# Kernel optimization log

Measured on AMD Instinct MI355X. Metric: run time of the kernel, lower is better.

## Reference

```python
import jax, jax.numpy as jnp
import numpy as np

NUM_LABELS = 64
START, END, PAD = 0, 1, 2
B, L, V, D = 128, 1024, 30000, 256


def make_transitions(key):
    # replicates CRF.init_weights
    t = jax.random.uniform(key, (NUM_LABELS, NUM_LABELS), minval=-0.1, maxval=0.1)
    t = t.at[:, START].set(-10000.0)
    t = t.at[END, :].set(-10000.0)
    t = t.at[PAD, :].set(-10000.0)
    t = t.at[:, PAD].set(-10000.0)
    t = t.at[PAD, PAD].set(0.0)
    t = t.at[PAD, END].set(0.0)
    return t.astype(jnp.float32)


def setup_inputs() -> dict:
    key = jax.random.key(0)
    k0, k1, k2, k3, k4 = jax.random.split(key, 5)
    x = jax.random.randint(k0, (B, L), 0, V)
    tags = jax.random.randint(k1, (B, L), 0, NUM_LABELS)
    mask = jnp.ones((B, L), dtype=jnp.float32)  # ignored by CRF (source passes mask=None)
    embed = jax.random.normal(k2, (V, D), dtype=jnp.float32)
    W = jax.random.normal(k3, (D, NUM_LABELS), dtype=jnp.float32) * 0.05
    b = jnp.zeros((NUM_LABELS,), dtype=jnp.float32)
    trans = make_transitions(k4)
    return {"x": x, "tags": tags, "mask": mask, "embed": embed, "W": W, "b": b, "trans": trans}


def _crf_nll(emissions, tags, trans):
    # emissions: [B, L, T]; tags: [B, L]; trans: [T, T]
    # NOTE: original CRF.forward ignores the user mask (passes mask=None ->
    # all-ones mask), so every position is valid and last tag is tags[:, -1].
    # gold path score
    e_scores = jnp.take_along_axis(emissions, tags[:, :, None], axis=2)[:, :, 0].sum(axis=1)
    t_scores = trans[tags[:, :-1], tags[:, 1:]].sum(axis=1)
    scores = e_scores + t_scores + trans[START, tags[:, 0]] + trans[tags[:, -1], END]
    # log partition: forward algorithm (log-space recursion over time)
    alpha0 = trans[START][None, :] + emissions[:, 0]  # [B, T]

    def step(alphas, emit_t):
        # alphas: [B, T_prev] -> logsumexp over previous tag
        new = jax.nn.logsumexp(alphas[:, :, None] + trans[None, :, :], axis=1) + emit_t
        return new, None

    alphas, _ = jax.lax.scan(step, alpha0, jnp.swapaxes(emissions[:, 1:], 0, 1))
    log_z = jax.nn.logsumexp(alphas + trans[:, END][None, :], axis=1)  # [B]
    return -jnp.sum(scores - log_z)


def reference(x, tags, mask, embed, W, b, trans):
    emissions = embed[x] @ W + b  # [B, L, T]
    return _crf_nll(emissions, tags, trans)
```

## Files before the change

kernel.cpp:

```cpp
#include <hip/hip_runtime.h>
#include <hip/hip_bf16.h>

#define B_ 128
#define L_ 1024
#define T_ 64
#define CSH 5
#define C_ 32

using short8 = __attribute__((ext_vector_type(8))) short;
using f32x4  = __attribute__((ext_vector_type(4))) float;
using f32x16 = __attribute__((ext_vector_type(16))) float;

static __device__ __forceinline__ unsigned short bfb(float x) {
  return __builtin_bit_cast(unsigned short, __float2bfloat16(x));
}
static __device__ __forceinline__ float asf(unsigned u) { return __builtin_bit_cast(float, u); }
static __device__ __forceinline__ float bf2f(unsigned short b) { return asf(((unsigned)b) << 16); }
static __device__ __forceinline__ unsigned pk2(float lo, float hi) {
  __hip_bfloat162 h = __float22bfloat162_rn(float2{lo, hi});
  unsigned u;
  __builtin_memcpy(&u, &h, 4);
  return u;
}
static __device__ __forceinline__ unsigned pk2t(float lo, float hi) {
  return __builtin_amdgcn_perm(__builtin_bit_cast(unsigned, hi),
                               __builtin_bit_cast(unsigned, lo), 0x07060302u);
}
static __device__ __forceinline__ void pswap(unsigned& x, unsigned& y) {
  asm("v_permlane32_swap_b32 %0, %1" : "+v"(x), "+v"(y));
}

__global__ __launch_bounds__(256) void k_prep(const float* __restrict__ W,
                                              unsigned short* __restrict__ Wswz,
                                              float* __restrict__ score,
                                              float* __restrict__ out) {
  if (blockIdx.x == 0) {
    if (threadIdx.x < 128) score[threadIdx.x] = 0.f;
    if (threadIdx.x == 0) out[0] = 0.f;
  }
  const int t = blockIdx.x * 256 + threadIdx.x;
  const int e = t * 4, k = e >> 6, n0 = e & 63;
  float4 w4 = *(const float4*)(W + e);
  const int base = ((k >> 5) << 11) + ((n0 >> 4) << 9) + (((k >> 3) & 3) << 7) +
                   ((n0 & 15) << 3) + (k & 7);
  Wswz[base + 0]  = bfb(w4.x);
  Wswz[base + 8]  = bfb(w4.y);
  Wswz[base + 16] = bfb(w4.z);
  Wswz[base + 24] = bfb(w4.w);
}

__global__ __launch_bounds__(256) void k_scan(const int* __restrict__ x,
                                              const int* __restrict__ tags,
                                              const float* __restrict__ embed,
                                              const unsigned short* __restrict__ Wswz,
                                              const float* __restrict__ bias,
                                              const float* __restrict__ trans,
                                              unsigned short* __restrict__ XT,
                                              float* __restrict__ rlog,
                                              float* __restrict__ score) {
  __shared__ __align__(16) unsigned short Ftile[4][2048];
  const int wv = threadIdx.x >> 6, L = threadIdx.x & 63;
  const int job = blockIdx.x * 4 + wv;
  const int c = job & (C_ - 1);
  const int b = job >> CSH;
  const int K = (1023 + C_ - 1) >> CSH;
  const int a = 1 + c * K;
  const int len = min(K, 1024 - a);
  const int nh = L & 31, hh = L >> 5;
  const int m = L & 15, q = L >> 4;
  unsigned short* Ft = Ftile[wv];
  const int* tg = tags + (size_t)b * L_;

  const float bj0 = bias[m], bj1 = bias[16 + m], bj2 = bias[32 + m], bj3 = bias[48 + m];
  for (int p = 0; p < 2; p++) {
    int tok = a + 16 * p + m;
    if (tok > 1023) tok = 1023;
    const float* er = embed + (size_t)x[b * 1024 + tok] * 256;
    f32x4 acc[4] = {{0.f,0.f,0.f,0.f},{0.f,0.f,0.f,0.f},{0.f,0.f,0.f,0.f},{0.f,0.f,0.f,0.f}};
#pragma unroll
    for (int kap = 0; kap < 8; kap++) {
      float4 p0 = *(const float4*)(er + 32 * kap + 8 * q);
      float4 p1 = *(const float4*)(er + 32 * kap + 8 * q + 4);
      unsigned u0 = pk2(p0.x, p0.y), u1 = pk2(p0.z, p0.w);
      unsigned u2 = pk2(p1.x, p1.y), u3 = pk2(p1.z, p1.w);
      short8 af = __builtin_bit_cast(short8, make_uint4(u0, u1, u2, u3));
#pragma unroll
      for (int u = 0; u < 4; u++) {
        short8 bf8 = *(const short8*)&Wswz[kap * 2048 + u * 512 + q * 128 + m * 8];
        acc[u] = __builtin_amdgcn_mfma_f32_16x16x32_bf16(af, bf8, acc[u], 0, 0, 0);
      }
    }
#pragma unroll
    for (int r = 0; r < 4; r++) {
      float e0 = acc[0][r] + bj0, e1 = acc[1][r] + bj1;
      float e2 = acc[2][r] + bj2, e3 = acc[3][r] + bj3;
      float mr = fmaxf(fmaxf(e0, e1), fmaxf(e2, e3));
#pragma unroll
      for (int off = 1; off < 16; off <<= 1) mr = fmaxf(mr, __shfl_xor(mr, off));
      float x0 = __expf(e0 - mr), x1 = __expf(e1 - mr);
      float x2 = __expf(e2 - mr), x3 = __expf(e3 - mr);
      float sr = (x0 + x1) + (x2 + x3);
#pragma unroll
      for (int off = 1; off < 16; off <<= 1) sr += __shfl_xor(sr, off);
      float rs = 1.0f / sr;
      const int row = 16 * p + 4 * q + r;
      Ft[row * 64 + m]      = bfb(x0 * rs);
      Ft[row * 64 + 16 + m] = bfb(x1 * rs);
      Ft[row * 64 + 32 + m] = bfb(x2 * rs);
      Ft[row * 64 + 48 + m] = bfb(x3 * rs);
    }
  }
  {
    float gold = 0.f;
    if (L < len) {
      const int tga = tg[a + L], tgp = tg[a - 1 + L];
      gold = __logf(bf2f(Ft[L * 64 + tga])) + trans[tgp * T_ + tga];
    }
#pragma unroll
    for (int off = 1; off < 64; off <<= 1) gold += __shfl_xor(gold, off);
    if (L == 0) atomicAdd(&score[b], gold);
  }

  short8 Af[2][4];
#pragma unroll
  for (int I = 0; I < 2; I++)
#pragma unroll
    for (int kap = 0; kap < 4; kap++) {
      short8 aa;
#pragma unroll
      for (int d = 0; d < 8; d++) {
        const int k = 16 * kap + 8 * hh + d;
        aa[d] = (short)bfb(__expf(trans[k * T_ + 32 * I + nh]));
      }
      Af[I][kap] = aa;
    }
  unsigned Bf[4][2][4];
#pragma unroll
  for (int kap = 0; kap < 4; kap++)
#pragma unroll
    for (int J = 0; J < 2; J++)
#pragma unroll
      for (int dw = 0; dw < 4; dw++) {
        int k0 = 16 * kap + 8 * hh + 2 * dw, n = 32 * J + nh;
        unsigned u = 0;
        if (k0 == n) u = 0x3F80u;
        if (k0 + 1 == n) u = 0x3F800000u;
        Bf[kap][J][dw] = u;
      }

  float logacc = 0.f;
  const f32x16 Z = {};
  for (int s = 0; s < len; s++) {
    uint2 Fc[2][4];
#pragma unroll
    for (int I = 0; I < 2; I++)
#pragma unroll
      for (int j = 0; j < 4; j++)
        Fc[I][j] = *(const uint2*)&Ft[s * 64 + (16 * I + 4 * j + 2 * hh) * 2];
    const bool rn = ((s & 15) == 15);
    float rs = 1.0f;
#pragma unroll
    for (int J = 0; J < 2; J++) {
      f32x16 D[2];
#pragma unroll
      for (int I = 0; I < 2; I++) {
        short8 b0 = __builtin_bit_cast(short8,
            make_uint4(Bf[0][J][0], Bf[0][J][1], Bf[0][J][2], Bf[0][J][3]));
        f32x16 d = __builtin_amdgcn_mfma_f32_32x32x16_bf16(Af[I][0], b0, Z, 0, 0, 0);
#pragma unroll
        for (int kap = 1; kap < 4; kap++) {
          short8 bk = __builtin_bit_cast(short8,
              make_uint4(Bf[kap][J][0], Bf[kap][J][1], Bf[kap][J][2], Bf[kap][J][3]));
          d = __builtin_amdgcn_mfma_f32_32x32x16_bf16(Af[I][kap], bk, d, 0, 0, 0);
        }
        D[I] = d;
      }
#pragma unroll
      for (int I = 0; I < 2; I++)
#pragma unroll
        for (int j = 0; j < 4; j++) {
          uint2 g = Fc[I][j];
          float f0 = asf(g.x << 16), f1 = asf(g.x & 0xffff0000u);
          float f2 = asf(g.y << 16), f3 = asf(g.y & 0xffff0000u);
          D[I][4 * j + 0] *= f0;
          D[I][4 * j + 1] *= f1;
          D[I][4 * j + 2] *= f2;
          D[I][4 * j + 3] *= f3;
        }
      if (rn) {
        if (J == 0) {
          float mx = D[0][0];
#pragma unroll
          for (int I = 0; I < 2; I++)
#pragma unroll
            for (int r = 0; r < 16; r++) mx = fmaxf(mx, D[I][r]);
#pragma unroll
          for (int off = 1; off < 64; off <<= 1) mx = fmaxf(mx, __shfl_xor(mx, off));
          rs = 1.0f / mx;
          logacc += __logf(mx);
        }
#pragma unroll
        for (int I = 0; I < 2; I++)
#pragma unroll
          for (int r = 0; r < 16; r++) D[I][r] *= rs;
      }
      unsigned PDt[2][4][2];
#pragma unroll
      for (int I = 0; I < 2; I++)
#pragma unroll
        for (int j = 0; j < 4; j++) {
          PDt[I][j][0] = pk2t(D[I][4 * j + 0], D[I][4 * j + 1]);
          PDt[I][j][1] = pk2t(D[I][4 * j + 2], D[I][4 * j + 3]);
        }
      if (s == len - 1) {
        unsigned short* Xrow = XT + (size_t)job * 4096 + 32 * J + nh;
#pragma unroll
        for (int I = 0; I < 2; I++)
#pragma unroll
          for (int j = 0; j < 4; j++)
#pragma unroll
            for (int pp = 0; pp < 2; pp++) {
              const int r = 32 * I + 8 * j + 4 * hh + 2 * pp;
              Xrow[(size_t)r * 64] = (unsigned short)(PDt[I][j][pp] & 0xffffu);
              Xrow[(size_t)(r + 1) * 64] = (unsigned short)(PDt[I][j][pp] >> 16);
            }
      } else {
#pragma unroll
        for (int kap = 0; kap < 4; kap++) {
          const int Ip = kap >> 1, e2 = 2 * (kap & 1);
          unsigned x0 = PDt[Ip][e2][0], y0 = PDt[Ip][e2 + 1][0];
          unsigned x1 = PDt[Ip][e2][1], y1 = PDt[Ip][e2 + 1][1];
          pswap(x0, y0);
          pswap(x1, y1);
          Bf[kap][J][0] = x0;
          Bf[kap][J][1] = x1;
          Bf[kap][J][2] = y0;
          Bf[kap][J][3] = y1;
        }
      }
    }
  }
  if (L == 0) rlog[job] = logacc;
}

__global__ __launch_bounds__(256) void k_tail(const unsigned short* __restrict__ XT,
                                              const float* __restrict__ rlog,
                                              const float* __restrict__ score,
                                              const int* __restrict__ x,
                                              const float* __restrict__ embed,
                                              const float* __restrict__ W,
                                              const float* __restrict__ bias,
                                              const float* __restrict__ trans,
                                              const int* __restrict__ tags,
                                              float* __restrict__ out) {
  __shared__ __align__(16) unsigned short Ptile[4][4096];
  __shared__ __align__(16) float vS[64];
  __shared__ float tlg[4];
  const int wv = threadIdx.x >> 6, L = threadIdx.x & 63;
  const int b = blockIdx.x;
  const int nh = L & 31, hh = L >> 5;
  const int* tg = tags + (size_t)b * L_;
  const f32x16 Z = {};
  unsigned Bf[4][2][4];

  const unsigned short* Sb = XT + (size_t)b * C_ * 4096;
  {
    float plog = 0.f;
#pragma unroll
    for (int kap = 0; kap < 4; kap++)
#pragma unroll
      for (int J = 0; J < 2; J++)
#pragma unroll
        for (int dw = 0; dw < 4; dw++) {
          int k0 = 16 * kap + 8 * hh + 2 * dw, n = 32 * J + nh;
          unsigned u = 0;
          if (k0 == n) u = 0x3F80u;
          if (k0 + 1 == n) u = 0x3F800000u;
          Bf[kap][J][dw] = u;
        }
    for (int r = 0; r < 8; r++) {
      short8 Ap[2][4];
#pragma unroll
      for (int I = 0; I < 2; I++)
#pragma unroll
        for (int kap = 0; kap < 4; kap++)
          Ap[I][kap] = *(const short8*)(Sb + (size_t)(8 * wv + r) * 4096 +
                                        (32 * I + nh) * 64 + 16 * kap + 8 * hh);
      const bool last = (r == 7);
      float rsw = 1.0f;
#pragma unroll
      for (int J = 0; J < 2; J++) {
        f32x16 D[2];
#pragma unroll
        for (int I = 0; I < 2; I++) {
          short8 b0 = __builtin_bit_cast(short8,
              make_uint4(Bf[0][J][0], Bf[0][J][1], Bf[0][J][2], Bf[0][J][3]));
          f32x16 d = __builtin_amdgcn_mfma_f32_32x32x16_bf16(Ap[I][0], b0, Z, 0, 0, 0);
#pragma unroll
          for (int kap = 1; kap < 4; kap++) {
            short8 bk = __builtin_bit_cast(short8,
                make_uint4(Bf[kap][J][0], Bf[kap][J][1], Bf[kap][J][2], Bf[kap][J][3]));
            d = __builtin_amdgcn_mfma_f32_32x32x16_bf16(Ap[I][kap], bk, d, 0, 0, 0);
          }
          D[I] = d;
        }
        if (J == 0) {
          float mx = D[0][0];
#pragma unroll
          for (int I = 0; I < 2; I++)
#pragma unroll
            for (int rr = 0; rr < 16; rr++) mx = fmaxf(mx, D[I][rr]);
#pragma unroll
          for (int off = 1; off < 64; off <<= 1) mx = fmaxf(mx, __shfl_xor(mx, off));
          mx = fmaxf(mx, 1e-30f);
          rsw = 1.0f / mx;
          plog += __logf(mx);
        }
#pragma unroll
        for (int I = 0; I < 2; I++)
#pragma unroll
          for (int rr = 0; rr < 16; rr++) D[I][rr] *= rsw;
        unsigned PDt[2][4][2];
#pragma unroll
        for (int I = 0; I < 2; I++)
#pragma unroll
          for (int j = 0; j < 4; j++) {
            PDt[I][j][0] = pk2t(D[I][4 * j + 0], D[I][4 * j + 1]);
            PDt[I][j][1] = pk2t(D[I][4 * j + 2], D[I][4 * j + 3]);
          }
        if (last) {
          unsigned short* Xrow = Ptile[wv] + 32 * J + nh;
#pragma unroll
          for (int I = 0; I < 2; I++)
#pragma unroll
            for (int j = 0; j < 4; j++)
#pragma unroll
              for (int pp = 0; pp < 2; pp++) {
                const int rr = 32 * I + 8 * j + 4 * hh + 2 * pp;
                Xrow[rr * 64] = (unsigned short)(PDt[I][j][pp] & 0xffffu);
                Xrow[(rr + 1) * 64] = (unsigned short)(PDt[I][j][pp] >> 16);
              }
        } else {
#pragma unroll
          for (int kap = 0; kap < 4; kap++) {
            const int Ip = kap >> 1, e2 = 2 * (kap & 1);
            unsigned x0 = PDt[Ip][e2][0], y0 = PDt[Ip][e2 + 1][0];
            unsigned x1 = PDt[Ip][e2][1], y1 = PDt[Ip][e2 + 1][1];
            pswap(x0, y0);
            pswap(x1, y1);
            Bf[kap][J][0] = x0;
            Bf[kap][J][1] = x1;
            Bf[kap][J][2] = y0;
            Bf[kap][J][3] = y1;
          }
        }
      }
    }
    if (L == 0) tlg[wv] = plog;
  }
  __syncthreads();
  if (threadIdx.x >= 64) return;

  float tlog = (tlg[0] + tlg[1]) + (tlg[2] + tlg[3]);
  {
#pragma unroll
    for (int kap = 0; kap < 4; kap++)
#pragma unroll
      for (int J = 0; J < 2; J++)
#pragma unroll
        for (int dw = 0; dw < 4; dw++) {
          int k0 = 16 * kap + 8 * hh + 2 * dw, n = 32 * J + nh;
          unsigned u = 0;
          if (k0 == n) u = 0x3F80u;
          if (k0 + 1 == n) u = 0x3F800000u;
          Bf[kap][J][dw] = u;
        }
    for (int r = 0; r < 4; r++) {
      short8 Ap[2][4];
#pragma unroll
      for (int I = 0; I < 2; I++)
#pragma unroll
        for (int kap = 0; kap < 4; kap++)
          Ap[I][kap] = *(const short8*)&Ptile[r][(32 * I + nh) * 64 + 16 * kap + 8 * hh];
      const bool last = (r == 3);
      float rsw = 1.0f;
#pragma unroll
      for (int J = 0; J < 2; J++) {
        f32x16 D[2];
#pragma unroll
        for (int I = 0; I < 2; I++) {
          short8 b0 = __builtin_bit_cast(short8,
              make_uint4(Bf[0][J][0], Bf[0][J][1], Bf[0][J][2], Bf[0][J][3]));
          f32x16 d = __builtin_amdgcn_mfma_f32_32x32x16_bf16(Ap[I][0], b0, Z, 0, 0, 0);
#pragma unroll
          for (int kap = 1; kap < 4; kap++) {
            short8 bk = __builtin_bit_cast(short8,
                make_uint4(Bf[kap][J][0], Bf[kap][J][1], Bf[kap][J][2], Bf[kap][J][3]));
            d = __builtin_amdgcn_mfma_f32_32x32x16_bf16(Ap[I][kap], bk, d, 0, 0, 0);
          }
          D[I] = d;
        }
        if (J == 0) {
          float mx = D[0][0];
#pragma unroll
          for (int I = 0; I < 2; I++)
#pragma unroll
            for (int rr = 0; rr < 16; rr++) mx = fmaxf(mx, D[I][rr]);
#pragma unroll
          for (int off = 1; off < 64; off <<= 1) mx = fmaxf(mx, __shfl_xor(mx, off));
          mx = fmaxf(mx, 1e-30f);
          rsw = 1.0f / mx;
          tlog += __logf(mx);
        }
#pragma unroll
        for (int I = 0; I < 2; I++)
#pragma unroll
          for (int rr = 0; rr < 16; rr++) D[I][rr] *= rsw;
        unsigned PDt[2][4][2];
#pragma unroll
        for (int I = 0; I < 2; I++)
#pragma unroll
          for (int j = 0; j < 4; j++) {
            PDt[I][j][0] = pk2t(D[I][4 * j + 0], D[I][4 * j + 1]);
            PDt[I][j][1] = pk2t(D[I][4 * j + 2], D[I][4 * j + 3]);
          }
        if (last) {
          unsigned short* Xrow = Ptile[0] + 32 * J + nh;
#pragma unroll
          for (int I = 0; I < 2; I++)
#pragma unroll
            for (int j = 0; j < 4; j++)
#pragma unroll
              for (int pp = 0; pp < 2; pp++) {
                const int rr = 32 * I + 8 * j + 4 * hh + 2 * pp;
                Xrow[rr * 64] = (unsigned short)(PDt[I][j][pp] & 0xffffu);
                Xrow[(rr + 1) * 64] = (unsigned short)(PDt[I][j][pp] >> 16);
              }
        } else {
#pragma unroll
          for (int kap = 0; kap < 4; kap++) {
            const int Ip = kap >> 1, e2 = 2 * (kap & 1);
            unsigned x0 = PDt[Ip][e2][0], y0 = PDt[Ip][e2 + 1][0];
            unsigned x1 = PDt[Ip][e2][1], y1 = PDt[Ip][e2 + 1][1];
            pswap(x0, y0);
            pswap(x1, y1);
            Bf[kap][J][0] = x0;
            Bf[kap][J][1] = x1;
            Bf[kap][J][2] = y0;
            Bf[kap][J][3] = y1;
          }
        }
      }
    }
  }

  const int i = L;
  const float* er0 = embed + (size_t)x[(size_t)b * L_] * 256;
  float e0 = bias[i], e1 = 0.f, e2 = 0.f, e3 = 0.f;
#pragma unroll 16
  for (int d = 0; d < 256; d += 4) {
    e0 = fmaf(er0[d + 0], W[(d + 0) * T_ + i], e0);
    e1 = fmaf(er0[d + 1], W[(d + 1) * T_ + i], e1);
    e2 = fmaf(er0[d + 2], W[(d + 2) * T_ + i], e2);
    e3 = fmaf(er0[d + 3], W[(d + 3) * T_ + i], e3);
  }
  float e = (e0 + e1) + (e2 + e3);
  float mr = e;
#pragma unroll
  for (int off = 1; off < 64; off <<= 1) mr = fmaxf(mr, __shfl_xor(mr, off));
  float pex = __expf(e - mr);
  float sr = pex;
#pragma unroll
  for (int off = 1; off < 64; off <<= 1) sr += __shfl_xor(sr, off);
  const int t0 = tg[0];
  float sc = score[b];
  sc += (__shfl(e, t0) - mr) - __logf(sr);
  sc += trans[t0] + trans[tg[L_ - 1] * T_ + 1];
  vS[i] = __expf(trans[i]) * (pex / sr);
  float rl = (i < 32) ? rlog[b * C_ + i] : 0.f;
#pragma unroll
  for (int off = 1; off < 64; off <<= 1) rl += __shfl_xor(rl, off);
  const uint4* Zr = (const uint4*)Ptile[0];
  uint4 Xr[8];
#pragma unroll
  for (int t = 0; t < 8; t++) Xr[t] = Zr[i * 8 + t];
  float a0 = 0.f, a1 = 0.f, a2 = 0.f, a3 = 0.f;
#pragma unroll
  for (int t = 0; t < 8; t++) {
    float4 va = *(const float4*)&vS[8 * t];
    float4 vb = *(const float4*)&vS[8 * t + 4];
    a0 = fmaf(asf(Xr[t].x << 16), va.x, a0);
    a1 = fmaf(asf(Xr[t].x & 0xffff0000u), va.y, a1);
    a2 = fmaf(asf(Xr[t].y << 16), va.z, a2);
    a3 = fmaf(asf(Xr[t].y & 0xffff0000u), va.w, a3);
    a0 = fmaf(asf(Xr[t].z << 16), vb.x, a0);
    a1 = fmaf(asf(Xr[t].z & 0xffff0000u), vb.y, a1);
    a2 = fmaf(asf(Xr[t].w << 16), vb.z, a2);
    a3 = fmaf(asf(Xr[t].w & 0xffff0000u), vb.w, a3);
  }
  float t2 = ((a0 + a1) + (a2 + a3)) * __expf(trans[i * T_ + 1]);
#pragma unroll
  for (int off = 1; off < 64; off <<= 1) t2 += __shfl_xor(t2, off);
  if (i == 0) {
    const float logz = rl + tlog + __logf(t2);
    atomicAdd(out, -(sc - logz));
  }
}

extern "C" void kernel_launch(void* const* d_in, const int* in_sizes, int n_in,
                              void* d_out, int out_size, void* d_ws, size_t ws_size,
                              hipStream_t stream) {
  const int* x = (const int*)d_in[0];
  const int* tags = (const int*)d_in[1];
  const float* embed = (const float*)d_in[3];
  const float* W = (const float*)d_in[4];
  const float* bias = (const float*)d_in[5];
  const float* trans = (const float*)d_in[6];

  char* ws = (char*)d_ws;
  unsigned short* XT = (unsigned short*)ws;
  float* rlog = (float*)(ws + (size_t)C_ * 1048576);
  float* score = (float*)((char*)rlog + 4096 * 4);
  unsigned short* Wswz = (unsigned short*)((char*)score + 128 * 4);
  float* out = (float*)d_out;

  k_prep<<<16, 256, 0, stream>>>(W, Wswz, score, out);
  k_scan<<<32 * C_, 256, 0, stream>>>(x, tags, embed, Wswz, bias, trans, XT, rlog, score);
  k_tail<<<B_, 256, 0, stream>>>(XT, rlog, score, x, embed, W, bias, trans, tags, out);
}
```

Baseline: 196.1 us.

## Store chunk products in MFMA B-fragment layout and combine chunks in reverse order

The scan kernel now writes each chunk's final transfer matrix as packed B-operand register fragments with coalesced uint4 stores, replacing scattered 2-byte transposed stores. The tail kernel combines chunks from last to first, using stored fragments directly as A operands with register double-buffered prefetch. The final vector product is folded into the last MFMA step, which removes the separate LDS readback. This relies on the reversed multiplication order and the reinterpreted layout being mathematically equivalent, and adds register pressure from the prefetch buffers.

```diff
diff --git a/kernel.cpp b/kernel.cpp
--- a/kernel.cpp
+++ b/kernel.cpp
@@ -55,7 +55,7 @@
                                               const unsigned short* __restrict__ Wswz,
                                               const float* __restrict__ bias,
                                               const float* __restrict__ trans,
-                                              unsigned short* __restrict__ XT,
+                                              uint4* __restrict__ XT,
                                               float* __restrict__ rlog,
                                               float* __restrict__ score) {
   __shared__ __align__(16) unsigned short Ftile[4][2048];
@@ -212,38 +212,33 @@
           PDt[I][j][0] = pk2t(D[I][4 * j + 0], D[I][4 * j + 1]);
           PDt[I][j][1] = pk2t(D[I][4 * j + 2], D[I][4 * j + 3]);
         }
-      if (s == len - 1) {
-        unsigned short* Xrow = XT + (size_t)job * 4096 + 32 * J + nh;
-#pragma unroll
-        for (int I = 0; I < 2; I++)
-#pragma unroll
-          for (int j = 0; j < 4; j++)
-#pragma unroll
-            for (int pp = 0; pp < 2; pp++) {
-              const int r = 32 * I + 8 * j + 4 * hh + 2 * pp;
-              Xrow[(size_t)r * 64] = (unsigned short)(PDt[I][j][pp] & 0xffffu);
-              Xrow[(size_t)(r + 1) * 64] = (unsigned short)(PDt[I][j][pp] >> 16);
-            }
-      } else {
-#pragma unroll
-        for (int kap = 0; kap < 4; kap++) {
-          const int Ip = kap >> 1, e2 = 2 * (kap & 1);
-          unsigned x0 = PDt[Ip][e2][0], y0 = PDt[Ip][e2 + 1][0];
-          unsigned x1 = PDt[Ip][e2][1], y1 = PDt[Ip][e2 + 1][1];
-          pswap(x0, y0);
-          pswap(x1, y1);
-          Bf[kap][J][0] = x0;
-          Bf[kap][J][1] = x1;
-          Bf[kap][J][2] = y0;
-          Bf[kap][J][3] = y1;
-        }
-      }
-    }
+#pragma unroll
+      for (int kap = 0; kap < 4; kap++) {
+        const int Ip = kap >> 1, e2 = 2 * (kap & 1);
+        unsigned x0 = PDt[Ip][e2][0], y0 = PDt[Ip][e2 + 1][0];
+        unsigned x1 = PDt[Ip][e2][1], y1 = PDt[Ip][e2 + 1][1];
+        pswap(x0, y0);
+        pswap(x1, y1);
+        Bf[kap][J][0] = x0;
+        Bf[kap][J][1] = x1;
+        Bf[kap][J][2] = y0;
+        Bf[kap][J][3] = y1;
+      }
+    }
+  }
+  {
+    uint4* Xj = XT + (size_t)job * 512 + L;
+#pragma unroll
+    for (int J = 0; J < 2; J++)
+#pragma unroll
+      for (int kap = 0; kap < 4; kap++)
+        Xj[(J * 4 + kap) * 64] =
+            make_uint4(Bf[kap][J][0], Bf[kap][J][1], Bf[kap][J][2], Bf[kap][J][3]);
   }
   if (L == 0) rlog[job] = logacc;
 }
 
-__global__ __launch_bounds__(256) void k_tail(const unsigned short* __restrict__ XT,
+__global__ __launch_bounds__(256) void k_tail(const uint4* __restrict__ XT,
                                               const float* __restrict__ rlog,
                                               const float* __restrict__ score,
                                               const int* __restrict__ x,
@@ -263,7 +258,7 @@
   const f32x16 Z = {};
   unsigned Bf[4][2][4];
 
-  const unsigned short* Sb = XT + (size_t)b * C_ * 4096;
+  const uint4* Sb4 = XT + ((size_t)(b * C_ + 8 * wv)) * 512 + L;
   {
     float plog = 0.f;
 #pragma unroll
@@ -278,15 +273,28 @@
           if (k0 + 1 == n) u = 0x3F800000u;
           Bf[kap][J][dw] = u;
         }
-    for (int r = 0; r < 8; r++) {
+    uint4 Aq[2][4], Aqn[2][4];
+#pragma unroll
+    for (int I = 0; I < 2; I++)
+#pragma unroll
+      for (int kap = 0; kap < 4; kap++)
+        Aq[I][kap] = Sb4[7 * 512 + (I * 4 + kap) * 64];
+    for (int rr = 0; rr < 8; rr++) {
+      const int r = 7 - rr;
+      if (r > 0) {
+#pragma unroll
+        for (int I = 0; I < 2; I++)
+#pragma unroll
+          for (int kap = 0; kap < 4; kap++)
+            Aqn[I][kap] = Sb4[(size_t)(r - 1) * 512 + (I * 4 + kap) * 64];
+      }
       short8 Ap[2][4];
 #pragma unroll
       for (int I = 0; I < 2; I++)
 #pragma unroll
         for (int kap = 0; kap < 4; kap++)
-          Ap[I][kap] = *(const short8*)(Sb + (size_t)(8 * wv + r) * 4096 +
-                                        (32 * I + nh) * 64 + 16 * kap + 8 * hh);
-      const bool last = (r == 7);
+          Ap[I][kap] = __builtin_bit_cast(short8, Aq[I][kap]);
+      const bool last = (r == 0);
       float rsw = 1.0f;
 #pragma unroll
       for (int J = 0; J < 2; J++) {
@@ -309,7 +317,7 @@
 #pragma unroll
           for (int I = 0; I < 2; I++)
 #pragma unroll
-            for (int rr = 0; rr < 16; rr++) mx = fmaxf(mx, D[I][rr]);
+            for (int rr2 = 0; rr2 < 16; rr2++) mx = fmaxf(mx, D[I][rr2]);
 #pragma unroll
           for (int off = 1; off < 64; off <<= 1) mx = fmaxf(mx, __shfl_xor(mx, off));
           mx = fmaxf(mx, 1e-30f);
@@ -319,7 +327,7 @@
 #pragma unroll
         for (int I = 0; I < 2; I++)
 #pragma unroll
-          for (int rr = 0; rr < 16; rr++) D[I][rr] *= rsw;
+          for (int rr2 = 0; rr2 < 16; rr2++) D[I][rr2] *= rsw;
         unsigned PDt[2][4][2];
 #pragma unroll
         for (int I = 0; I < 2; I++)
@@ -336,9 +344,9 @@
             for (int j = 0; j < 4; j++)
 #pragma unroll
               for (int pp = 0; pp < 2; pp++) {
-                const int rr = 32 * I + 8 * j + 4 * hh + 2 * pp;
-                Xrow[rr * 64] = (unsigned short)(PDt[I][j][pp] & 0xffffu);
-                Xrow[(rr + 1) * 64] = (unsigned short)(PDt[I][j][pp] >> 16);
+                const int rw = 32 * I + 8 * j + 4 * hh + 2 * pp;
+                Xrow[rw * 64] = (unsigned short)(PDt[I][j][pp] & 0xffffu);
+                Xrow[(rw + 1) * 64] = (unsigned short)(PDt[I][j][pp] >> 16);
               }
         } else {
 #pragma unroll
@@ -355,6 +363,13 @@
           }
         }
       }
+      if (r > 0) {
+#pragma unroll
+        for (int I = 0; I < 2; I++)
+#pragma unroll
+          for (int kap = 0; kap < 4; kap++)
+            Aq[I][kap] = Aqn[I][kap];
+      }
     }
     if (L == 0) tlg[wv] = plog;
   }
@@ -362,97 +377,6 @@
   if (threadIdx.x >= 64) return;
 
   float tlog = (tlg[0] + tlg[1]) + (tlg[2] + tlg[3]);
-  {
-#pragma unroll
-    for (int kap = 0; kap < 4; kap++)
-#pragma unroll
-      for (int J = 0; J < 2; J++)
-#pragma unroll
-        for (int dw = 0; dw < 4; dw++) {
-          int k0 = 16 * kap + 8 * hh + 2 * dw, n = 32 * J + nh;
-          unsigned u = 0;
-          if (k0 == n) u = 0x3F80u;
-          if (k0 + 1 == n) u = 0x3F800000u;
-          Bf[kap][J][dw] = u;
-        }
-    for (int r = 0; r < 4; r++) {
-      short8 Ap[2][4];
-#pragma unroll
-      for (int I = 0; I < 2; I++)
-#pragma unroll
-        for (int kap = 0; kap < 4; kap++)
-          Ap[I][kap] = *(const short8*)&Ptile[r][(32 * I + nh) * 64 + 16 * kap + 8 * hh];
-      const bool last = (r == 3);
-      float rsw = 1.0f;
-#pragma unroll
-      for (int J = 0; J < 2; J++) {
-        f32x16 D[2];
-#pragma unroll
-        for (int I = 0; I < 2; I++) {
-          short8 b0 = __builtin_bit_cast(short8,
-              make_uint4(Bf[0][J][0], Bf[0][J][1], Bf[0][J][2], Bf[0][J][3]));
-          f32x16 d = __builtin_amdgcn_mfma_f32_32x32x16_bf16(Ap[I][0], b0, Z, 0, 0, 0);
-#pragma unroll
-          for (int kap = 1; kap < 4; kap++) {
-            short8 bk = __builtin_bit_cast(short8,
-                make_uint4(Bf[kap][J][0], Bf[kap][J][1], Bf[kap][J][2], Bf[kap][J][3]));
-            d = __builtin_amdgcn_mfma_f32_32x32x16_bf16(Ap[I][kap], bk, d, 0, 0, 0);
-          }
-          D[I] = d;
-        }
-        if (J == 0) {
-          float mx = D[0][0];
-#pragma unroll
-          for (int I = 0; I < 2; I++)
-#pragma unroll
-            for (int rr = 0; rr < 16; rr++) mx = fmaxf(mx, D[I][rr]);
-#pragma unroll
-          for (int off = 1; off < 64; off <<= 1) mx = fmaxf(mx, __shfl_xor(mx, off));
-          mx = fmaxf(mx, 1e-30f);
-          rsw = 1.0f / mx;
-          tlog += __logf(mx);
-        }
-#pragma unroll
-        for (int I = 0; I < 2; I++)
-#pragma unroll
-          for (int rr = 0; rr < 16; rr++) D[I][rr] *= rsw;
-        unsigned PDt[2][4][2];
-#pragma unroll
-        for (int I = 0; I < 2; I++)
-#pragma unroll
-          for (int j = 0; j < 4; j++) {
-            PDt[I][j][0] = pk2t(D[I][4 * j + 0], D[I][4 * j + 1]);
-            PDt[I][j][1] = pk2t(D[I][4 * j + 2], D[I][4 * j + 3]);
-          }
-        if (last) {
-          unsigned short* Xrow = Ptile[0] + 32 * J + nh;
-#pragma unroll
-          for (int I = 0; I < 2; I++)
-#pragma unroll
-            for (int j = 0; j < 4; j++)
-#pragma unroll
-              for (int pp = 0; pp < 2; pp++) {
-                const int rr = 32 * I + 8 * j + 4 * hh + 2 * pp;
-                Xrow[rr * 64] = (unsigned short)(PDt[I][j][pp] & 0xffffu);
-                Xrow[(rr + 1) * 64] = (unsigned short)(PDt[I][j][pp] >> 16);
-              }
-        } else {
-#pragma unroll
-          for (int kap = 0; kap < 4; kap++) {
-            const int Ip = kap >> 1, e2 = 2 * (kap & 1);
-            unsigned x0 = PDt[Ip][e2][0], y0 = PDt[Ip][e2 + 1][0];
-            unsigned x1 = PDt[Ip][e2][1], y1 = PDt[Ip][e2 + 1][1];
-            pswap(x0, y0);
-            pswap(x1, y1);
-            Bf[kap][J][0] = x0;
-            Bf[kap][J][1] = x1;
-            Bf[kap][J][2] = y0;
-            Bf[kap][J][3] = y1;
-          }
-        }
-      }
-    }
-  }
 
   const int i = L;
   const float* er0 = embed + (size_t)x[(size_t)b * L_] * 256;
@@ -480,25 +404,97 @@
   float rl = (i < 32) ? rlog[b * C_ + i] : 0.f;
 #pragma unroll
   for (int off = 1; off < 64; off <<= 1) rl += __shfl_xor(rl, off);
-  const uint4* Zr = (const uint4*)Ptile[0];
-  uint4 Xr[8];
-#pragma unroll
-  for (int t = 0; t < 8; t++) Xr[t] = Zr[i * 8 + t];
-  float a0 = 0.f, a1 = 0.f, a2 = 0.f, a3 = 0.f;
-#pragma unroll
-  for (int t = 0; t < 8; t++) {
-    float4 va = *(const float4*)&vS[8 * t];
-    float4 vb = *(const float4*)&vS[8 * t + 4];
-    a0 = fmaf(asf(Xr[t].x << 16), va.x, a0);
-    a1 = fmaf(asf(Xr[t].x & 0xffff0000u), va.y, a1);
-    a2 = fmaf(asf(Xr[t].y << 16), va.z, a2);
-    a3 = fmaf(asf(Xr[t].y & 0xffff0000u), va.w, a3);
-    a0 = fmaf(asf(Xr[t].z << 16), vb.x, a0);
-    a1 = fmaf(asf(Xr[t].z & 0xffff0000u), vb.y, a1);
-    a2 = fmaf(asf(Xr[t].w << 16), vb.z, a2);
-    a3 = fmaf(asf(Xr[t].w & 0xffff0000u), vb.w, a3);
-  }
-  float t2 = ((a0 + a1) + (a2 + a3)) * __expf(trans[i * T_ + 1]);
+
+  float tacc = 0.f;
+  {
+#pragma unroll
+    for (int kap = 0; kap < 4; kap++)
+#pragma unroll
+      for (int J = 0; J < 2; J++)
+#pragma unroll
+        for (int dw = 0; dw < 4; dw++) {
+          int k0 = 16 * kap + 8 * hh + 2 * dw, n = 32 * J + nh;
+          unsigned u = 0;
+          if (k0 == n) u = 0x3F80u;
+          if (k0 + 1 == n) u = 0x3F800000u;
+          Bf[kap][J][dw] = u;
+        }
+    for (int rr = 0; rr < 4; rr++) {
+      const int r = 3 - rr;
+      short8 Ap[2][4];
+#pragma unroll
+      for (int I = 0; I < 2; I++)
+#pragma unroll
+        for (int kap = 0; kap < 4; kap++)
+          Ap[I][kap] = *(const short8*)&Ptile[r][(32 * I + nh) * 64 + 16 * kap + 8 * hh];
+      const bool last = (r == 0);
+      float rsw = 1.0f;
+#pragma unroll
+      for (int J = 0; J < 2; J++) {
+        f32x16 D[2];
+#pragma unroll
+        for (int I = 0; I < 2; I++) {
+          short8 b0 = __builtin_bit_cast(short8,
+              make_uint4(Bf[0][J][0], Bf[0][J][1], Bf[0][J][2], Bf[0][J][3]));
+          f32x16 d = __builtin_amdgcn_mfma_f32_32x32x16_bf16(Ap[I][0], b0, Z, 0, 0, 0);
+#pragma unroll
+          for (int kap = 1; kap < 4; kap++) {
+            short8 bk = __builtin_bit_cast(short8,
+                make_uint4(Bf[kap][J][0], Bf[kap][J][1], Bf[kap][J][2], Bf[kap][J][3]));
+            d = __builtin_amdgcn_mfma_f32_32x32x16_bf16(Ap[I][kap], bk, d, 0, 0, 0);
+          }
+          D[I] = d;
+        }
+        if (J == 0) {
+          float mx = D[0][0];
+#pragma unroll
+          for (int I = 0; I < 2; I++)
+#pragma unroll
+            for (int rr2 = 0; rr2 < 16; rr2++) mx = fmaxf(mx, D[I][rr2]);
+#pragma unroll
+          for (int off = 1; off < 64; off <<= 1) mx = fmaxf(mx, __shfl_xor(mx, off));
+          mx = fmaxf(mx, 1e-30f);
+          rsw = 1.0f / mx;
+          tlog += __logf(mx);
+        }
+#pragma unroll
+        for (int I = 0; I < 2; I++)
+#pragma unroll
+          for (int rr2 = 0; rr2 < 16; rr2++) D[I][rr2] *= rsw;
+        if (last) {
+          float dJ = 0.f;
+#pragma unroll
+          for (int I = 0; I < 2; I++)
+#pragma unroll
+            for (int r2 = 0; r2 < 16; r2++)
+              dJ = fmaf(D[I][r2], vS[32 * I + (r2 & 3) + 8 * (r2 >> 2) + 4 * hh], dJ);
+          tacc = fmaf(__expf(trans[(32 * J + nh) * T_ + 1]), dJ, tacc);
+        } else {
+          unsigned PDt[2][4][2];
+#pragma unroll
+          for (int I = 0; I < 2; I++)
+#pragma unroll
+            for (int j = 0; j < 4; j++) {
+              PDt[I][j][0] = pk2t(D[I][4 * j + 0], D[I][4 * j + 1]);
+              PDt[I][j][1] = pk2t(D[I][4 * j + 2], D[I][4 * j + 3]);
+            }
+#pragma unroll
+          for (int kap = 0; kap < 4; kap++) {
+            const int Ip = kap >> 1, e2b = 2 * (kap & 1);
+            unsigned x0 = PDt[Ip][e2b][0], y0 = PDt[Ip][e2b + 1][0];
+            unsigned x1 = PDt[Ip][e2b][1], y1 = PDt[Ip][e2b + 1][1];
+            pswap(x0, y0);
+            pswap(x1, y1);
+            Bf[kap][J][0] = x0;
+            Bf[kap][J][1] = x1;
+            Bf[kap][J][2] = y0;
+            Bf[kap][J][3] = y1;
+          }
+        }
+      }
+    }
+  }
+  float t2 = tacc;
 #pragma unroll
   for (int off = 1; off < 64; off <<= 1) t2 += __shfl_xor(t2, off);
   if (i == 0) {
@@ -518,7 +514,7 @@
   const float* trans = (const float*)d_in[6];
 
   char* ws = (char*)d_ws;
-  unsigned short* XT = (unsigned short*)ws;
+  uint4* XT = (uint4*)ws;
   float* rlog = (float*)(ws + (size_t)C_ * 1048576);
   float* score = (float*)((char*)rlog + 4096 * 4);
   unsigned short* Wswz = (unsigned short*)((char*)score + 128 * 4);
```

New measurement: 191.7 us. 2.2% less time.
